# Kernel tuning notes

Measured on AMD Instinct MI355X. Metric: run time of the kernel, lower is better.

Reference implementation:

```python
import jax, jax.numpy as jnp
import numpy as np
from jax import lax


def haar_dwt2(x):
    """Level-1 Haar (db1) 2D DWT on [N, H, W] with even H, W.
    Returns cA, cH, cV (cD is discarded by the module), each [N, H//2, W//2].
    Matches pywt/ptwt db1 block form: cA=(a+b+c+d)/2, etc."""
    a = x[:, 0::2, 0::2]
    b = x[:, 0::2, 1::2]
    c = x[:, 1::2, 0::2]
    d = x[:, 1::2, 1::2]
    cA = (a + b + c + d) * 0.5
    cH = (a + b - c - d) * 0.5  # horizontal detail (highpass along rows axis)
    cV = (a - b + c - d) * 0.5  # vertical detail (highpass along cols axis)
    return cA, cH, cV


def conv2d_same(x, w, b):
    # x: [N, Cin, H, W], w: [Cout, Cin, kh, kw]
    y = lax.conv_general_dilated(x, w, window_strides=(1, 1), padding='SAME',
                                 dimension_numbers=('NCHW', 'OIHW', 'NCHW'))
    return y + b[None, :, None, None]


def maxpool2(x):
    return lax.reduce_window(x, -jnp.inf, lax.max,
                             window_dimensions=(1, 1, 2, 2),
                             window_strides=(1, 1, 2, 2), padding='VALID')


def setup_inputs() -> dict:
    key = jax.random.key(0)
    ks = jax.random.split(key, 7)
    B, C, H, W = 32, 3, 512, 512
    x = jax.random.normal(ks[0], (B, C, H, W), dtype=jnp.float32)
    # conv stack params (Conv2d(1,16,3), Conv2d(16,8,3), Conv2d(8,4,1))
    w1 = jax.random.normal(ks[1], (16, 1, 3, 3), dtype=jnp.float32) * (1.0 / 3.0)
    b1 = jnp.zeros((16,), dtype=jnp.float32)
    w2 = jax.random.normal(ks[2], (8, 16, 3, 3), dtype=jnp.float32) * (1.0 / 12.0)
    b2 = jnp.zeros((8,), dtype=jnp.float32)
    w3 = jax.random.normal(ks[3], (4, 8, 1, 1), dtype=jnp.float32) * (1.0 / 2.83)
    b3 = jnp.zeros((4,), dtype=jnp.float32)
    return {"x": x, "w1": w1, "b1": b1, "w2": w2, "b2": b2, "w3": w3, "b3": b3}


def reference(x, w1, b1, w2, b2, w3, b3):
    B, C, H, W = x.shape
    # Batch the per-image/per-channel loop: treat each channel as one map.
    flat = x.reshape(B * C, H, W)
    cA, cH, cV = haar_dwt2(flat)  # [B*C, H/2, W/2]

    # Low-frequency conv stack on approx coeffs (1 input channel per map).
    h = cA[:, None, :, :]                       # [B*C, 1, H/2, W/2]
    h = maxpool2(jax.nn.relu(conv2d_same(h, w1, b1)))
    h = maxpool2(jax.nn.relu(conv2d_same(h, w2, b2)))
    h = conv2d_same(h, w3, b3)                  # [B*C, 4, H/8, W/8]
    # per-channel flatten, then concat over channels (dim=1 in the original)
    low = h.reshape(B, 1, -1)                   # [B, 1, C*4*(H/8)*(W/8)]

    # High-frequency: per channel concat [cH.flatten(), cV.flatten()],
    # then concat over channels.
    n = (H // 2) * (W // 2)
    high = jnp.concatenate([cH.reshape(B, C, n), cV.reshape(B, C, n)], axis=-1)
    high = high.reshape(B, 1, C * 2 * n)        # [B, 1, C*2*(H/2)*(W/2)]
    return low, high
```

## Files before the change

### kernel.cpp

```cpp
#include <hip/hip_runtime.h>


typedef float v2f __attribute__((ext_vector_type(2)));

#define PK_FMA_W0(acc, w, d) \
    asm("v_pk_fma_f32 %0, %1, %2, %0 op_sel:[0,0,0] op_sel_hi:[1,0,1]" \
        : "+v"(acc) : "s"(w), "v"(d))
#define PK_FMA_W1(acc, w, d) \
    asm("v_pk_fma_f32 %0, %1, %2, %0 op_sel:[0,1,0] op_sel_hi:[1,1,1]" \
        : "+v"(acc) : "s"(w), "v"(d))
#define PK_MUL_W0(dst, w, d) \
    asm("v_pk_mul_f32 %0, %1, %2 op_sel:[0,0] op_sel_hi:[1,0]" \
        : "=v"(dst) : "s"(w), "v"(d))
#define PK_MUL_W1(dst, w, d) \
    asm("v_pk_mul_f32 %0, %1, %2 op_sel:[0,1] op_sel_hi:[1,1]" \
        : "=v"(dst) : "s"(w), "v"(d))

__global__ __launch_bounds__(256, 4) void fused_all_kernel(
    const float* __restrict__ x,
    const float* __restrict__ w1, const float* __restrict__ b1,
    const float* __restrict__ w2, const float* __restrict__ b2,
    const float* __restrict__ w3, const float* __restrict__ b3,
    float* __restrict__ outLow, float* __restrict__ outHigh)
{
    __shared__ __align__(16) float ca[70 * 72];
    __shared__ __align__(16) float h1s[4 * 34 * 36];

    int img = blockIdx.x >> 4;
    int t   = blockIdx.x & 15;
    int ty = t >> 2, tx = t & 3;
    int hy0 = ty * 32 - 1, hx0 = tx * 32 - 1;
    int cy0 = ty * 64 - 3, cx0 = tx * 64 - 3;

    const float* xi = x + img * 262144;
    float* hb = outHigh + img * 131072;

    #pragma unroll
    for (int k = 0; k < 4; ++k) {
        int i = threadIdx.x + k * 256;
        int row = i >> 4, cg = i & 15;
        int gy = ty * 64 + row;
        int gx = tx * 64 + cg * 4;
        const float* r0 = xi + (2 * gy) * 512 + 2 * gx;
        const float* r1 = r0 + 512;
        float4 t0 = *(const float4*)(r0);
        float4 t1 = *(const float4*)(r0 + 4);
        float4 u0 = *(const float4*)(r1);
        float4 u1 = *(const float4*)(r1 + 4);
        float4 vA, vH, vV;
        vA.x = (t0.x + t0.y + u0.x + u0.y) * 0.5f;
        vH.x = (t0.x + t0.y - u0.x - u0.y) * 0.5f;
        vV.x = (t0.x - t0.y + u0.x - u0.y) * 0.5f;
        vA.y = (t0.z + t0.w + u0.z + u0.w) * 0.5f;
        vH.y = (t0.z + t0.w - u0.z - u0.w) * 0.5f;
        vV.y = (t0.z - t0.w + u0.z - u0.w) * 0.5f;
        vA.z = (t1.x + t1.y + u1.x + u1.y) * 0.5f;
        vH.z = (t1.x + t1.y - u1.x - u1.y) * 0.5f;
        vV.z = (t1.x - t1.y + u1.x - u1.y) * 0.5f;
        vA.w = (t1.z + t1.w + u1.z + u1.w) * 0.5f;
        vH.w = (t1.z + t1.w - u1.z - u1.w) * 0.5f;
        vV.w = (t1.z - t1.w + u1.z - u1.w) * 0.5f;
        int po = (gy << 8) + gx;
        *(float4*)(hb + po) = vH;
        *(float4*)(hb + 65536 + po) = vV;
        float* cp = ca + (row + 3) * 72 + cg * 4 + 3;
        cp[0] = vA.x; cp[1] = vA.y; cp[2] = vA.z; cp[3] = vA.w;
    }

    for (int i = threadIdx.x; i < 804; i += 256) {
        int r, c;
        if (i < 210)      { r = i / 70;              c = i - r * 70; }
        else if (i < 420) { int j = i - 210; r = 67 + j / 70; c = j - (j / 70) * 70; }
        else              { int j = i - 420; r = 3 + j / 6; int k6 = j - (j / 6) * 6;
                            c = (k6 < 3) ? k6 : (64 + k6); }
        int gy = cy0 + r, gx = cx0 + c;
        float v = 0.f;
        if ((unsigned)gy < 256u && (unsigned)gx < 256u) {
            const float* p0 = xi + (2 * gy) * 512 + 2 * gx;
            float2 a = *(const float2*)(p0);
            float2 b = *(const float2*)(p0 + 512);
            v = (a.x + a.y + b.x + b.y) * 0.5f;
        }
        ca[r * 72 + c] = v;
    }

    int ly = threadIdx.x >> 4, lx = threadIdx.x & 15;

    v2f acc2[4][2][2];
    #pragma unroll
    for (int o2 = 0; o2 < 4; ++o2)
        #pragma unroll
        for (int r = 0; r < 2; ++r)
            #pragma unroll
            for (int c = 0; c < 2; ++c) acc2[o2][r][c] = (v2f){0.f, 0.f};

    __syncthreads();

    #pragma unroll 1
    for (int cc = 0; cc < 4; ++cc) {
        v2f wp1[2][9];
        #pragma unroll
        for (int o2 = 0; o2 < 2; ++o2)
            #pragma unroll
            for (int k = 0; k < 9; ++k)
                wp1[o2][k] = (v2f){ w1[(cc * 4 + o2 * 2    ) * 9 + k],
                                    w1[(cc * 4 + o2 * 2 + 1) * 9 + k] };
        if (cc) __syncthreads();

        #pragma unroll 1
        for (int k5 = 0; k5 < 5; ++k5) {
            int i = threadIdx.x + k5 * 256;
            if (i < 1156) {
                int hy = i / 34, hx = i - hy * 34;
                const float* pb = ca + (2 * hy) * 72 + 2 * hx;
                v2f pr[4][2];
                #pragma unroll
                for (int r = 0; r < 4; ++r) {
                    pr[r][0] = *(const v2f*)(pb + r * 72);
                    pr[r][1] = *(const v2f*)(pb + r * 72 + 2);
                }
                bool oob = ((unsigned)(hy0 + hy) >= 128u) | ((unsigned)(hx0 + hx) >= 128u);
                v2f am[2][4];
                #pragma unroll
                for (int ky = 0; ky < 3; ++ky)
                #pragma unroll
                for (int kx = 0; kx < 3; ++kx) {
                    #pragma unroll
                    for (int o2 = 0; o2 < 2; ++o2)
                    #pragma unroll
                    for (int dy = 0; dy < 2; ++dy)
                    #pragma unroll
                    for (int dx = 0; dx < 2; ++dx) {
                        v2f d = pr[ky + dy][(kx + dx) >> 1];
                        if (ky == 0 && kx == 0) {
                            if (((kx + dx) & 1) == 0) PK_MUL_W0(am[o2][dy * 2 + dx], wp1[o2][0], d);
                            else                      PK_MUL_W1(am[o2][dy * 2 + dx], wp1[o2][0], d);
                        } else {
                            if (((kx + dx) & 1) == 0) PK_FMA_W0(am[o2][dy * 2 + dx], wp1[o2][ky * 3 + kx], d);
                            else                      PK_FMA_W1(am[o2][dy * 2 + dx], wp1[o2][ky * 3 + kx], d);
                        }
                    }
                }
                #pragma unroll
                for (int o2 = 0; o2 < 2; ++o2) {
                    float mx = fmaxf(fmaxf(am[o2][0].x, am[o2][1].x),
                                     fmaxf(am[o2][2].x, am[o2][3].x));
                    float my = fmaxf(fmaxf(am[o2][0].y, am[o2][1].y),
                                     fmaxf(am[o2][2].y, am[o2][3].y));
                    mx = fmaxf(mx + b1[cc * 4 + o2 * 2    ], 0.f);
                    my = fmaxf(my + b1[cc * 4 + o2 * 2 + 1], 0.f);
                    h1s[((o2 * 2    ) * 34 + hy) * 36 + hx] = oob ? 0.f : mx;
                    h1s[((o2 * 2 + 1) * 34 + hy) * 36 + hx] = oob ? 0.f : my;
                }
            }
        }
        __syncthreads();

        #pragma unroll
        for (int icl = 0; icl < 4; ++icl) {
            const float* base = h1s + (icl * 34 + ly * 2) * 36 + lx * 2;
            v2f wr[4][2];
            #pragma unroll
            for (int r = 0; r < 4; ++r) {
                wr[r][0] = *(const v2f*)(base + r * 36);
                wr[r][1] = *(const v2f*)(base + r * 36 + 2);
            }
            int ic = cc * 4 + icl;
            #pragma unroll
            for (int ky = 0; ky < 3; ++ky)
            #pragma unroll
            for (int kx = 0; kx < 3; ++kx)
            #pragma unroll
            for (int o2 = 0; o2 < 4; ++o2) {
                v2f wv = (v2f){ w2[((o2 * 2    ) * 16 + ic) * 9 + ky * 3 + kx],
                                w2[((o2 * 2 + 1) * 16 + ic) * 9 + ky * 3 + kx] };
                #pragma unroll
                for (int r = 0; r < 2; ++r)
                #pragma unroll
                for (int c = 0; c < 2; ++c) {
                    v2f d = wr[r + ky][(c + kx) >> 1];
                    if (((c + kx) & 1) == 0) PK_FMA_W0(acc2[o2][r][c], wv, d);
                    else                     PK_FMA_W1(acc2[o2][r][c], wv, d);
                }
            }
        }
    }

    float h2v[8];
    #pragma unroll
    for (int o2 = 0; o2 < 4; ++o2) {
        float mx = fmaxf(fmaxf(acc2[o2][0][0].x, acc2[o2][0][1].x),
                         fmaxf(acc2[o2][1][0].x, acc2[o2][1][1].x));
        float my = fmaxf(fmaxf(acc2[o2][0][0].y, acc2[o2][0][1].y),
                         fmaxf(acc2[o2][1][0].y, acc2[o2][1][1].y));
        h2v[o2 * 2    ] = fmaxf(mx + b2[o2 * 2    ], 0.f);
        h2v[o2 * 2 + 1] = fmaxf(my + b2[o2 * 2 + 1], 0.f);
    }
    float* dst = outLow + img * 16384;
    int pos = (ty * 16 + ly) * 64 + tx * 16 + lx;
    #pragma unroll
    for (int oc3 = 0; oc3 < 4; ++oc3) {
        float s = b3[oc3];
        #pragma unroll
        for (int ic = 0; ic < 8; ++ic) s += w3[oc3 * 8 + ic] * h2v[ic];
        dst[oc3 * 4096 + pos] = s;
    }
}

extern "C" void kernel_launch(void* const* d_in, const int* in_sizes, int n_in,
                              void* d_out, int out_size, void* d_ws, size_t ws_size,
                              hipStream_t stream) {
    const float* x  = (const float*)d_in[0];
    const float* w1 = (const float*)d_in[1];
    const float* b1 = (const float*)d_in[2];
    const float* w2 = (const float*)d_in[3];
    const float* b2 = (const float*)d_in[4];
    const float* w3 = (const float*)d_in[5];
    const float* b3 = (const float*)d_in[6];
    float* out     = (float*)d_out;
    float* outLow  = out;
    float* outHigh = out + 1572864;

    fused_all_kernel<<<1536, 256, 0, stream>>>(x, w1, b1, w2, b2, w3, b3,
                                               outLow, outHigh);
}
```

Before: 218.4 us.

## Halve tile height and split conv2 output channels across thread halves

Each image is now split into 32 tiles instead of 16, so the launch has twice as many blocks and each block uses less shared memory. The 256 threads are divided into two groups of 128, and each group computes 4 of the 8 conv2 output channels. The intermediate results are exchanged through shared memory so the 1x1 conv3 can use all 8 channels. The launch bound is raised to allow 6 blocks per unit and improve occupancy. In exchange, the halo is recomputed relative to a smaller tile, and the kernel gains two extra barriers plus a shared-memory exchange.

```diff
diff --git a/kernel.cpp b/kernel.cpp
--- a/kernel.cpp
+++ b/kernel.cpp
@@ -16,31 +16,31 @@
     asm("v_pk_mul_f32 %0, %1, %2 op_sel:[0,1] op_sel_hi:[1,1]" \
         : "=v"(dst) : "s"(w), "v"(d))
 
-__global__ __launch_bounds__(256, 4) void fused_all_kernel(
+__global__ __launch_bounds__(256, 6) void fused_all_kernel(
     const float* __restrict__ x,
     const float* __restrict__ w1, const float* __restrict__ b1,
     const float* __restrict__ w2, const float* __restrict__ b2,
     const float* __restrict__ w3, const float* __restrict__ b3,
     float* __restrict__ outLow, float* __restrict__ outHigh)
 {
-    __shared__ __align__(16) float ca[70 * 72];
-    __shared__ __align__(16) float h1s[4 * 34 * 36];
-
-    int img = blockIdx.x >> 4;
-    int t   = blockIdx.x & 15;
-    int ty = t >> 2, tx = t & 3;
-    int hy0 = ty * 32 - 1, hx0 = tx * 32 - 1;
-    int cy0 = ty * 64 - 3, cx0 = tx * 64 - 3;
+    __shared__ __align__(16) float ca[38 * 72];
+    __shared__ __align__(16) float h1s[4 * 18 * 36];
+
+    int img = blockIdx.x >> 5;
+    int t   = blockIdx.x & 31;
+    int tyy = t >> 2, txx = t & 3;
+    int hy0 = tyy * 16 - 1, hx0 = txx * 32 - 1;
+    int cy0 = tyy * 32 - 3, cx0 = txx * 64 - 3;
 
     const float* xi = x + img * 262144;
     float* hb = outHigh + img * 131072;
 
     #pragma unroll
-    for (int k = 0; k < 4; ++k) {
+    for (int k = 0; k < 2; ++k) {
         int i = threadIdx.x + k * 256;
         int row = i >> 4, cg = i & 15;
-        int gy = ty * 64 + row;
-        int gx = tx * 64 + cg * 4;
+        int gy = tyy * 32 + row;
+        int gx = txx * 64 + cg * 4;
         const float* r0 = xi + (2 * gy) * 512 + 2 * gx;
         const float* r1 = r0 + 512;
         float4 t0 = *(const float4*)(r0);
@@ -67,10 +67,10 @@
         cp[0] = vA.x; cp[1] = vA.y; cp[2] = vA.z; cp[3] = vA.w;
     }
 
-    for (int i = threadIdx.x; i < 804; i += 256) {
+    for (int i = threadIdx.x; i < 612; i += 256) {
         int r, c;
         if (i < 210)      { r = i / 70;              c = i - r * 70; }
-        else if (i < 420) { int j = i - 210; r = 67 + j / 70; c = j - (j / 70) * 70; }
+        else if (i < 420) { int j = i - 210; r = 35 + j / 70; c = j - (j / 70) * 70; }
         else              { int j = i - 420; r = 3 + j / 6; int k6 = j - (j / 6) * 6;
                             c = (k6 < 3) ? k6 : (64 + k6); }
         int gy = cy0 + r, gx = cx0 + c;
@@ -84,11 +84,13 @@
         ca[r * 72 + c] = v;
     }
 
-    int ly = threadIdx.x >> 4, lx = threadIdx.x & 15;
-
-    v2f acc2[4][2][2];
-    #pragma unroll
-    for (int o2 = 0; o2 < 4; ++o2)
+    int pos = threadIdx.x & 127;
+    int ocg = __builtin_amdgcn_readfirstlane(threadIdx.x >> 7);
+    int ly = pos >> 4, lx = pos & 15;
+
+    v2f acc2[2][2][2];
+    #pragma unroll
+    for (int o2 = 0; o2 < 2; ++o2)
         #pragma unroll
         for (int r = 0; r < 2; ++r)
             #pragma unroll
@@ -108,9 +110,9 @@
         if (cc) __syncthreads();
 
         #pragma unroll 1
-        for (int k5 = 0; k5 < 5; ++k5) {
+        for (int k5 = 0; k5 < 3; ++k5) {
             int i = threadIdx.x + k5 * 256;
-            if (i < 1156) {
+            if (i < 612) {
                 int hy = i / 34, hx = i - hy * 34;
                 const float* pb = ca + (2 * hy) * 72 + 2 * hx;
                 v2f pr[4][2];
@@ -149,8 +151,8 @@
                                      fmaxf(am[o2][2].y, am[o2][3].y));
                     mx = fmaxf(mx + b1[cc * 4 + o2 * 2    ], 0.f);
                     my = fmaxf(my + b1[cc * 4 + o2 * 2 + 1], 0.f);
-                    h1s[((o2 * 2    ) * 34 + hy) * 36 + hx] = oob ? 0.f : mx;
-                    h1s[((o2 * 2 + 1) * 34 + hy) * 36 + hx] = oob ? 0.f : my;
+                    h1s[((o2 * 2    ) * 18 + hy) * 36 + hx] = oob ? 0.f : mx;
+                    h1s[((o2 * 2 + 1) * 18 + hy) * 36 + hx] = oob ? 0.f : my;
                 }
             }
         }
@@ -158,7 +160,7 @@
 
         #pragma unroll
         for (int icl = 0; icl < 4; ++icl) {
-            const float* base = h1s + (icl * 34 + ly * 2) * 36 + lx * 2;
+            const float* base = h1s + (icl * 18 + ly * 2) * 36 + lx * 2;
             v2f wr[4][2];
             #pragma unroll
             for (int r = 0; r < 4; ++r) {
@@ -171,9 +173,10 @@
             #pragma unroll
             for (int kx = 0; kx < 3; ++kx)
             #pragma unroll
-            for (int o2 = 0; o2 < 4; ++o2) {
-                v2f wv = (v2f){ w2[((o2 * 2    ) * 16 + ic) * 9 + ky * 3 + kx],
-                                w2[((o2 * 2 + 1) * 16 + ic) * 9 + ky * 3 + kx] };
+            for (int o2 = 0; o2 < 2; ++o2) {
+                int oc0 = ocg * 4 + o2 * 2;
+                v2f wv = (v2f){ w2[((oc0    ) * 16 + ic) * 9 + ky * 3 + kx],
+                                w2[((oc0 + 1) * 16 + ic) * 9 + ky * 3 + kx] };
                 #pragma unroll
                 for (int r = 0; r < 2; ++r)
                 #pragma unroll
@@ -186,24 +189,35 @@
         }
     }
 
-    float h2v[8];
-    #pragma unroll
-    for (int o2 = 0; o2 < 4; ++o2) {
+    float h2v[4];
+    #pragma unroll
+    for (int o2 = 0; o2 < 2; ++o2) {
         float mx = fmaxf(fmaxf(acc2[o2][0][0].x, acc2[o2][0][1].x),
                          fmaxf(acc2[o2][1][0].x, acc2[o2][1][1].x));
         float my = fmaxf(fmaxf(acc2[o2][0][0].y, acc2[o2][0][1].y),
                          fmaxf(acc2[o2][1][0].y, acc2[o2][1][1].y));
-        h2v[o2 * 2    ] = fmaxf(mx + b2[o2 * 2    ], 0.f);
-        h2v[o2 * 2 + 1] = fmaxf(my + b2[o2 * 2 + 1], 0.f);
-    }
+        h2v[o2 * 2    ] = fmaxf(mx + b2[ocg * 4 + o2 * 2    ], 0.f);
+        h2v[o2 * 2 + 1] = fmaxf(my + b2[ocg * 4 + o2 * 2 + 1], 0.f);
+    }
+    __syncthreads();
+    float* hx2 = h1s;
+    #pragma unroll
+    for (int j = 0; j < 4; ++j) hx2[pos * 9 + ocg * 4 + j] = h2v[j];
+    __syncthreads();
+
+    float hv[8];
+    #pragma unroll
+    for (int ic = 0; ic < 8; ++ic) hv[ic] = hx2[pos * 9 + ic];
     float* dst = outLow + img * 16384;
-    int pos = (ty * 16 + ly) * 64 + tx * 16 + lx;
-    #pragma unroll
-    for (int oc3 = 0; oc3 < 4; ++oc3) {
+    int posg = (tyy * 8 + ly) * 64 + txx * 16 + lx;
+    int o3g = ocg;
+    #pragma unroll
+    for (int jo = 0; jo < 2; ++jo) {
+        int oc3 = o3g * 2 + jo;
         float s = b3[oc3];
         #pragma unroll
-        for (int ic = 0; ic < 8; ++ic) s += w3[oc3 * 8 + ic] * h2v[ic];
-        dst[oc3 * 4096 + pos] = s;
+        for (int ic = 0; ic < 8; ++ic) s += w3[oc3 * 8 + ic] * hv[ic];
+        dst[oc3 * 4096 + posg] = s;
     }
 }
 
@@ -221,6 +235,6 @@
     float* outLow  = out;
     float* outHigh = out + 1572864;
 
-    fused_all_kernel<<<1536, 256, 0, stream>>>(x, w1, b1, w2, b2, w3, b3,
+    fused_all_kernel<<<3072, 256, 0, stream>>>(x, w1, b1, w2, b2, w3, b3,
                                                outLow, outHigh);
 }
```

After: 209.7 us. 4.0% less time.
